# Optimization experiments

Measured on AMD Instinct MI355X. Metric: run time of the kernel, lower is better.

Reference implementation:

```python
import jax, jax.numpy as jnp
import numpy as np

HEAD_SIZE = 64

def setup_inputs() -> dict:
    key = jax.random.key(0)
    k1, k2, k3, k4 = jax.random.split(key, 4)
    B, T, D = 4, 4096, 768
    x = jax.random.normal(k1, (B, T, D), dtype=jnp.float32)
    Wq = jax.random.normal(k2, (D, HEAD_SIZE), dtype=jnp.float32) * (1.0 / np.sqrt(D))
    Wk = jax.random.normal(k3, (D, HEAD_SIZE), dtype=jnp.float32) * (1.0 / np.sqrt(D))
    Wv = jax.random.normal(k4, (D, HEAD_SIZE), dtype=jnp.float32) * (1.0 / np.sqrt(D))
    return {"x": x, "Wq": Wq, "Wk": Wk, "Wv": Wv}

def reference(x, Wq, Wk, Wv):
    # q,k,v: [B, T, H]
    q = jnp.einsum('btd,dh->bth', x, Wq)
    k = jnp.einsum('btd,dh->bth', x, Wk)
    v = jnp.einsum('btd,dh->bth', x, Wv)
    # scores: [B, T, T]; causal mask via lower-triangular band, -inf elsewhere
    scores = jnp.einsum('bqh,bkh->bqk', q, k)
    T = x.shape[1]
    causal = jnp.tril(jnp.ones((T, T), dtype=bool))  # band_part(ones, -1, 0)
    scores = jnp.where(causal[None, :, :], scores, -jnp.inf)
    attn = jax.nn.softmax(scores / np.sqrt(HEAD_SIZE), axis=-1)
    # dropout is identity in eval mode
    return jnp.einsum('bqk,bkh->bqh', attn, v)
```

## Files before the change

kernel.cpp:

```cpp
#include <hip/hip_runtime.h>
#include <math.h>

typedef __attribute__((ext_vector_type(8))) short short8;
typedef __attribute__((ext_vector_type(4))) float f32x4;
typedef unsigned short ushort_t;

#define TSEQ   4096
#define NBATCH 4
#define DMODEL 768
#define HS     64
#define KSPLIT 8

static __device__ __forceinline__ ushort_t f2bf(float f) {
  union { float f; unsigned u; } v; v.f = f;
  unsigned r = v.u + 0x7fffu + ((v.u >> 16) & 1u);
  return (ushort_t)(r >> 16);
}
static __device__ __forceinline__ float bf2f(ushort_t u) {
  union { unsigned u; float f; } v; v.u = ((unsigned)u) << 16; return v.f;
}

#define MFMA16(a,b,c) __builtin_amdgcn_mfma_f32_16x16x32_bf16((a),(b),(c),0,0,0)

__global__ __launch_bounds__(256) void wprep(
    const float* __restrict__ Wq, const float* __restrict__ Wk,
    const float* __restrict__ Wv, ushort_t* __restrict__ Wt)
{
  __shared__ float lds[64 * 65];
  const int m = blockIdx.x / 12, kc = blockIdx.x % 12, k0 = kc * 64;
  const float* W = (m == 0) ? Wq : (m == 1) ? Wk : Wv;
  const int tid = threadIdx.x;
#pragma unroll
  for (int i = 0; i < 16; i++) {
    const int row = i * 4 + (tid >> 6), col = tid & 63;
    lds[row * 65 + col] = W[(size_t)(k0 + row) * HS + col];
  }
  __syncthreads();
#pragma unroll
  for (int i = 0; i < 16; i++) {
    const int n = i * 4 + (tid >> 6), kk = tid & 63;
    Wt[(size_t)(m * 64 + n) * DMODEL + k0 + kk] = f2bf(lds[kk * 65 + n]);
  }
}

__global__ __launch_bounds__(512, 1) void qkv_mfma(
    const float* __restrict__ x, const ushort_t* __restrict__ Wt,
    ushort_t* __restrict__ q, ushort_t* __restrict__ kO, ushort_t* __restrict__ vT)
{
  __shared__ __align__(16) ushort_t sA[2][64 * 72];
  __shared__ __align__(16) ushort_t sB[2][192 * 64];

  const int tid  = threadIdx.x;
  const int w    = tid >> 6;
  const int wm   = w >> 2, wn = w & 3;
  const int lane = tid & 63;
  const int l16  = lane & 15, quad = lane >> 4;
  const int M0   = blockIdx.x * 64;

  const int arow = tid >> 3, acol = (tid & 7) * 8;
  const float* ax = x + (size_t)(M0 + arow) * DMODEL + acol;

  const int bcol_l = lane >> 3;
  const int bkoff  = (((lane & 7) ^ (bcol_l & 7)) << 3);

  f32x4 acc[2][3];
#pragma unroll
  for (int mt = 0; mt < 2; mt++)
#pragma unroll
    for (int nt = 0; nt < 3; nt++) acc[mt][nt] = (f32x4){0.f, 0.f, 0.f, 0.f};

  {
#pragma unroll
    for (int j = 0; j < 3; j++) {
      const int colb = w * 24 + j * 8;
      __builtin_amdgcn_global_load_lds(
          (const __attribute__((address_space(1))) ushort_t*)
              (Wt + (size_t)(colb + bcol_l) * DMODEL + bkoff),
          (__attribute__((address_space(3))) ushort_t*)(&sB[0][colb * 64]),
          16, 0, 0);
    }
    const float4 f0 = *(const float4*)(ax);
    const float4 f1 = *(const float4*)(ax + 4);
    short8 p;
    p[0]=f2bf(f0.x); p[1]=f2bf(f0.y); p[2]=f2bf(f0.z); p[3]=f2bf(f0.w);
    p[4]=f2bf(f1.x); p[5]=f2bf(f1.y); p[6]=f2bf(f1.z); p[7]=f2bf(f1.w);
    *(short8*)(&sA[0][arow * 72 + acol]) = p;
  }

  for (int ks = 0; ks < DMODEL / 64; ks++) {
    const int cur = ks & 1, nxt = cur ^ 1;
    __syncthreads();

    float4 f0n, f1n;
    if (ks < DMODEL / 64 - 1) {
#pragma unroll
      for (int j = 0; j < 3; j++) {
        const int colb = w * 24 + j * 8;
        __builtin_amdgcn_global_load_lds(
            (const __attribute__((address_space(1))) ushort_t*)
                (Wt + (size_t)(colb + bcol_l) * DMODEL + (ks + 1) * 64 + bkoff),
            (__attribute__((address_space(3))) ushort_t*)(&sB[nxt][colb * 64]),
            16, 0, 0);
      }
      f0n = *(const float4*)(ax + (ks + 1) * 64);
      f1n = *(const float4*)(ax + (ks + 1) * 64 + 4);
    }

    const ushort_t* sAc = &sA[cur][0];
    const ushort_t* sBc = &sB[cur][0];
#pragma unroll
    for (int kc = 0; kc < 2; kc++) {
      const short8 a0 = *(const short8*)(sAc + (wm * 32 + l16)      * 72 + kc * 32 + quad * 8);
      const short8 a1 = *(const short8*)(sAc + (wm * 32 + 16 + l16) * 72 + kc * 32 + quad * 8);
      const int kswz = (kc * 32 + quad * 8) ^ ((l16 & 7) << 3);
#pragma unroll
      for (int nt = 0; nt < 3; nt++) {
        const short8 bf =
            *(const short8*)(sBc + (wn * 48 + nt * 16 + l16) * 64 + kswz);
        acc[0][nt] = MFMA16(a0, bf, acc[0][nt]);
        acc[1][nt] = MFMA16(a1, bf, acc[1][nt]);
      }
    }

    if (ks < DMODEL / 64 - 1) {
      short8 p;
      p[0]=f2bf(f0n.x); p[1]=f2bf(f0n.y); p[2]=f2bf(f0n.z); p[3]=f2bf(f0n.w);
      p[4]=f2bf(f1n.x); p[5]=f2bf(f1n.y); p[6]=f2bf(f1n.z); p[7]=f2bf(f1n.w);
      *(short8*)(&sA[nxt][arow * 72 + acol]) = p;
    }
  }

#pragma unroll
  for (int mt = 0; mt < 2; mt++)
#pragma unroll
    for (int nt = 0; nt < 3; nt++) {
      const int gnt = wn * 3 + nt;
      const int mat = gnt >> 2;
      if (mat == 0) {
        const int col = (gnt & 3) * 16 + l16;
#pragma unroll
        for (int r = 0; r < 4; r++)
          q[(size_t)(M0 + wm * 32 + mt * 16 + quad * 4 + r) * HS + col] =
              f2bf(acc[mt][nt][r] * 0.125f);
      } else if (mat == 1) {
        const int cb2 = (gnt & 3) * 2 + (l16 >> 3);
#pragma unroll
        for (int r = 0; r < 4; r++) {
          const int trow  = M0 + wm * 32 + mt * 16 + quad * 4 + r;
          const int cphys = ((cb2 ^ (trow & 7)) << 3) | (l16 & 7);
          kO[(size_t)trow * HS + cphys] = f2bf(acc[mt][nt][r]);
        }
      }
    }
  __syncthreads();
  float* vls = (float*)&sA[0][0];
#pragma unroll
  for (int mt = 0; mt < 2; mt++)
#pragma unroll
    for (int nt = 0; nt < 3; nt++) {
      const int gnt = wn * 3 + nt;
      if ((gnt >> 2) == 2) {
        const int vcol = (gnt & 3) * 16 + l16;
#pragma unroll
        for (int r = 0; r < 4; r++)
          vls[(wm * 32 + mt * 16 + quad * 4 + r) * 65 + vcol] = acc[mt][nt][r];
      }
    }
  __syncthreads();
  const int d = tid >> 3, seg = tid & 7;
  short8 pk;
#pragma unroll
  for (int i = 0; i < 8; i++) pk[i] = (short)f2bf(vls[(seg * 8 + i) * 65 + d]);
  {
    const int tb  = M0 & (TSEQ - 1);
    const int kbp = seg ^ (d & 7);
    *(short8*)(vT + ((size_t)(M0 >> 12) * HS + d) * TSEQ + tb + kbp * 8) = pk;
  }
}

__global__ __launch_bounds__(256, 4) void attn_part(
    const ushort_t* __restrict__ q, const ushort_t* __restrict__ k,
    const ushort_t* __restrict__ vT, float* __restrict__ ML, ushort_t* __restrict__ OP)
{
  __shared__ __align__(16) ushort_t sK[2][64 * 64];
  __shared__ __align__(16) ushort_t sV[2][64 * 64];
  __shared__ __align__(16) ushort_t sP[4][16 * 64];

  const int idx  = blockIdx.x;
  const int s    = idx & 7;
  const int b    = (idx >> 3) & 3;
  const int jp   = idx >> 5;
  const int tid  = threadIdx.x;
  const int w    = tid >> 6;
  const int lane = tid & 63;
  const int l16  = lane & 15, quad = lane >> 4;

  const ushort_t* qg = q  + (size_t)b * TSEQ * HS;
  const ushort_t* kg = k  + (size_t)b * TSEQ * HS;
  const ushort_t* vg = vT + (size_t)b * HS * TSEQ;

  const int srow = lane >> 3;
  const int scol = (lane & 7) * 8;

#pragma unroll
  for (int h = 0; h < 2; h++) {
    const int j  = h ? jp : (63 - jp);
    const int R0 = j * 64 + w * 16;

    const short8 qf0 = *(const short8*)(qg + (size_t)(R0 + l16) * HS +      quad * 8);
    const short8 qf1 = *(const short8*)(qg + (size_t)(R0 + l16) * HS + 32 + quad * 8);

    f32x4 o[4];
#pragma unroll
    for (int dt = 0; dt < 4; dt++) o[dt] = (f32x4){0.f, 0.f, 0.f, 0.f};
    float mrow = -INFINITY, lrow = 0.f;

    const int nkt = j + 1;
    int kt = s, cur = 0;
    if (h) __syncthreads();
    if (kt < nkt) {
      const int k0 = kt * 64;
#pragma unroll
      for (int jj = 0; jj < 2; jj++) {
        const int r0 = w * 16 + jj * 8;
        __builtin_amdgcn_global_load_lds(
            (const __attribute__((address_space(1))) ushort_t*)
                (kg + (size_t)(k0 + r0 + srow) * HS + scol),
            (__attribute__((address_space(3))) ushort_t*)(&sK[0][r0 * 64]),
            16, 0, 0);
        __builtin_amdgcn_global_load_lds(
            (const __attribute__((address_space(1))) ushort_t*)
                (vg + (size_t)(r0 + srow) * TSEQ + k0 + scol),
            (__attribute__((address_space(3))) ushort_t*)(&sV[0][r0 * 64]),
            16, 0, 0);
      }
    }
    for (; kt < nkt; kt += KSPLIT) {
      const int k0 = kt * 64;
      __syncthreads();
      if (kt + KSPLIT < nkt) {
        const int kn = (kt + KSPLIT) * 64;
#pragma unroll
        for (int jj = 0; jj < 2; jj++) {
          const int r0 = w * 16 + jj * 8;
          __builtin_amdgcn_global_load_lds(
              (const __attribute__((address_space(1))) ushort_t*)
                  (kg + (size_t)(kn + r0 + srow) * HS + scol),
              (__attribute__((address_space(3))) ushort_t*)(&sK[cur ^ 1][r0 * 64]),
              16, 0, 0);
          __builtin_amdgcn_global_load_lds(
              (const __attribute__((address_space(1))) ushort_t*)
                  (vg + (size_t)(r0 + srow) * TSEQ + kn + scol),
              (__attribute__((address_space(3))) ushort_t*)(&sV[cur ^ 1][r0 * 64]),
              16, 0, 0);
        }
      }
      const ushort_t* sKc = &sK[cur][0];
      const ushort_t* sVc = &sV[cur][0];
      const int sw = (l16 & 7) << 3;

      f32x4 sT[4];
      __builtin_amdgcn_s_setprio(1);
#pragma unroll
      for (int ct = 0; ct < 4; ct++) {
        sT[ct] = (f32x4){0.f, 0.f, 0.f, 0.f};
        const short8 kfa = *(const short8*)(sKc + (ct * 16 + l16) * 64 + ((quad * 8)      ^ sw));
        const short8 kfb = *(const short8*)(sKc + (ct * 16 + l16) * 64 + ((32 + quad * 8) ^ sw));
        sT[ct] = MFMA16(kfa, qf0, sT[ct]);
        sT[ct] = MFMA16(kfb, qf1, sT[ct]);
      }
      __builtin_amdgcn_s_setprio(0);
      if (k0 + 63 > R0) {
        const int qrow = R0 + l16;
#pragma unroll
        for (int ct = 0; ct < 4; ct++)
#pragma unroll
          for (int r = 0; r < 4; r++)
            sT[ct][r] = (k0 + ct * 16 + quad * 4 + r <= qrow) ? sT[ct][r] : -INFINITY;
      }
      float tm = -INFINITY;
#pragma unroll
      for (int ct = 0; ct < 4; ct++)
#pragma unroll
        for (int r = 0; r < 4; r++) tm = fmaxf(tm, sT[ct][r]);
      tm = fmaxf(tm, __shfl_xor(tm, 16));
      tm = fmaxf(tm, __shfl_xor(tm, 32));
      const float mn = fmaxf(mrow, tm);
      const float al = __expf(mrow - mn);
      mrow = mn;
      float ps = 0.f;
#pragma unroll
      for (int ct = 0; ct < 4; ct++)
#pragma unroll
        for (int r = 0; r < 4; r++) { sT[ct][r] = __expf(sT[ct][r] - mn); ps += sT[ct][r]; }
      ps += __shfl_xor(ps, 16);
      ps += __shfl_xor(ps, 32);
      lrow = lrow * al + ps;
      ushort_t* Pw = &sP[w][0];
#pragma unroll
      for (int ct = 0; ct < 4; ct++) {
        ushort4 pk;
        pk.x = f2bf(sT[ct][0]); pk.y = f2bf(sT[ct][1]);
        pk.z = f2bf(sT[ct][2]); pk.w = f2bf(sT[ct][3]);
        const int pb = (ct * 2 + (quad >> 1)) ^ (l16 & 7);
        *(ushort4*)(Pw + l16 * 64 + pb * 8 + (quad & 1) * 4) = pk;
      }
      float alo[4];
#pragma unroll
      for (int r = 0; r < 4; r++) alo[r] = __shfl(al, quad * 4 + r);
#pragma unroll
      for (int dt = 0; dt < 4; dt++)
#pragma unroll
        for (int r = 0; r < 4; r++) o[dt][r] *= alo[r];
      const short8 pf0 = *(const short8*)(Pw + l16 * 64 + (((quad)     ^ (l16 & 7)) << 3));
      const short8 pf1 = *(const short8*)(Pw + l16 * 64 + (((4 + quad) ^ (l16 & 7)) << 3));
      __builtin_amdgcn_s_setprio(1);
#pragma unroll
      for (int dt = 0; dt < 4; dt++) {
        const short8 vfa = *(const short8*)(sVc + (dt * 16 + l16) * 64 + ((quad * 8)      ^ sw));
        const short8 vfb = *(const short8*)(sVc + (dt * 16 + l16) * 64 + ((32 + quad * 8) ^ sw));
        o[dt] = MFMA16(pf0, vfa, o[dt]);
        o[dt] = MFMA16(pf1, vfb, o[dt]);
      }
      __builtin_amdgcn_s_setprio(0);
      cur ^= 1;
    }

    const size_t base = ((size_t)(b * KSPLIT + s) * TSEQ);
    if (quad == 0) {
      ML[(base + R0 + l16) * 2 + 0] = mrow;
      ML[(base + R0 + l16) * 2 + 1] = lrow;
    }
#pragma unroll
    for (int dt = 0; dt < 4; dt++)
#pragma unroll
      for (int r = 0; r < 4; r++)
        OP[(base + R0 + quad * 4 + r) * HS + dt * 16 + l16] = f2bf(o[dt][r]);
  }
}

__global__ __launch_bounds__(256) void attn_merge(
    const float* __restrict__ ML, const ushort_t* __restrict__ OP,
    float* __restrict__ out)
{
  const int row = blockIdx.x * 32 + (threadIdx.x >> 3);
  const int b   = row >> 12, t = row & (TSEQ - 1);
  const int d0  = (threadIdx.x & 7) * 8;
  float m[KSPLIT], l[KSPLIT];
  float M = -INFINITY;
#pragma unroll
  for (int ss = 0; ss < KSPLIT; ss++) {
    const size_t i = ((size_t)(b * KSPLIT + ss) * TSEQ + t);
    m[ss] = ML[i * 2]; l[ss] = ML[i * 2 + 1];
    M = fmaxf(M, m[ss]);
  }
  float den = 0.f;
  float n0=0.f,n1=0.f,n2=0.f,n3=0.f,n4=0.f,n5=0.f,n6=0.f,n7=0.f;
#pragma unroll
  for (int ss = 0; ss < KSPLIT; ss++) {
    const float a = __expf(m[ss] - M);
    den += l[ss] * a;
    const size_t i = ((size_t)(b * KSPLIT + ss) * TSEQ + t);
    const short8 u = *(const short8*)(OP + i * HS + d0);
    n0 += a * bf2f((ushort_t)u[0]); n1 += a * bf2f((ushort_t)u[1]);
    n2 += a * bf2f((ushort_t)u[2]); n3 += a * bf2f((ushort_t)u[3]);
    n4 += a * bf2f((ushort_t)u[4]); n5 += a * bf2f((ushort_t)u[5]);
    n6 += a * bf2f((ushort_t)u[6]); n7 += a * bf2f((ushort_t)u[7]);
  }
  const float inv = 1.f / den;
  float* op = out + (size_t)row * HS + d0;
  *(float4*)(op)     = make_float4(n0 * inv, n1 * inv, n2 * inv, n3 * inv);
  *(float4*)(op + 4) = make_float4(n4 * inv, n5 * inv, n6 * inv, n7 * inv);
}

extern "C" void kernel_launch(void* const* d_in, const int* in_sizes, int n_in,
                              void* d_out, int out_size, void* d_ws, size_t ws_size,
                              hipStream_t stream) {
  const float* x  = (const float*)d_in[0];
  const float* Wq = (const float*)d_in[1];
  const float* Wk = (const float*)d_in[2];
  const float* Wv = (const float*)d_in[3];
  float* out = (float*)d_out;

  char* ws = (char*)d_ws;
  ushort_t* Wt = (ushort_t*)ws;
  ushort_t* qb = (ushort_t*)(ws + 294912);
  ushort_t* kb = (ushort_t*)(ws + 294912 + 2097152);
  ushort_t* vb = (ushort_t*)(ws + 294912 + 2 * 2097152);
  float*    ml = (float*)   (ws + 294912 + 3 * 2097152);
  ushort_t* op = (ushort_t*)(ws + 294912 + 3 * 2097152 + 1048576);

  wprep<<<36, 256, 0, stream>>>(Wq, Wk, Wv, Wt);
  qkv_mfma<<<(NBATCH * TSEQ) / 64, 512, 0, stream>>>(x, Wt, qb, kb, vb);
  attn_part<<<32 * NBATCH * KSPLIT, 256, 0, stream>>>(qb, kb, vb, ml, op);
  attn_merge<<<512, 256, 0, stream>>>(ml, op, out);
}
```

Measured before the change: 128.5 us.

## Process two 64-row query groups per block to reuse each K/V tile

Each attention block now handles a 128-row query tile, split into two 64-row groups, and applies every staged K/V tile in LDS to both groups. Global K/V traffic and tile staging per query row roughly halve, and the grid shrinks to half as many blocks. In exchange the kernel holds twice the accumulator and Q registers and twice the P scratch, and occupancy is lowered to 3 waves per SIMD. Fewer blocks may also leave CUs idle or load-imbalanced.

New measurement: 132.2 us. +2.9%, slower.

```diff
diff --git a/kernel.cpp b/kernel.cpp
--- a/kernel.cpp
+++ b/kernel.cpp
@@ -178,13 +178,13 @@
   }
 }
 
-__global__ __launch_bounds__(256, 4) void attn_part(
+__global__ __launch_bounds__(256, 3) void attn_part(
     const ushort_t* __restrict__ q, const ushort_t* __restrict__ k,
     const ushort_t* __restrict__ vT, float* __restrict__ ML, ushort_t* __restrict__ OP)
 {
   __shared__ __align__(16) ushort_t sK[2][64 * 64];
   __shared__ __align__(16) ushort_t sV[2][64 * 64];
-  __shared__ __align__(16) ushort_t sP[4][16 * 64];
+  __shared__ __align__(16) ushort_t sP[4][2][16 * 64];
 
   const int idx  = blockIdx.x;
   const int s    = idx & 7;
@@ -204,18 +204,26 @@
 
 #pragma unroll
   for (int h = 0; h < 2; h++) {
-    const int j  = h ? jp : (63 - jp);
-    const int R0 = j * 64 + w * 16;
-
-    const short8 qf0 = *(const short8*)(qg + (size_t)(R0 + l16) * HS +      quad * 8);
-    const short8 qf1 = *(const short8*)(qg + (size_t)(R0 + l16) * HS + 32 + quad * 8);
-
-    f32x4 o[4];
-#pragma unroll
-    for (int dt = 0; dt < 4; dt++) o[dt] = (f32x4){0.f, 0.f, 0.f, 0.f};
-    float mrow = -INFINITY, lrow = 0.f;
-
-    const int nkt = j + 1;
+    const int j  = h ? jp : (31 - jp);
+    const int TB = j * 128;
+
+    short8 qf[2][2];
+#pragma unroll
+    for (int g = 0; g < 2; g++) {
+      const int R0g = TB + g * 64 + w * 16;
+      qf[g][0] = *(const short8*)(qg + (size_t)(R0g + l16) * HS +      quad * 8);
+      qf[g][1] = *(const short8*)(qg + (size_t)(R0g + l16) * HS + 32 + quad * 8);
+    }
+
+    f32x4 o[2][4];
+#pragma unroll
+    for (int g = 0; g < 2; g++)
+#pragma unroll
+      for (int dt = 0; dt < 4; dt++) o[g][dt] = (f32x4){0.f, 0.f, 0.f, 0.f};
+    float mrow[2] = {-INFINITY, -INFINITY};
+    float lrow[2] = {0.f, 0.f};
+
+    const int nkt = 2 * j + 2;
     int kt = s, cur = 0;
     if (h) __syncthreads();
     if (kt < nkt) {
@@ -259,83 +267,93 @@
       const ushort_t* sVc = &sV[cur][0];
       const int sw = (l16 & 7) << 3;
 
-      f32x4 sT[4];
-      __builtin_amdgcn_s_setprio(1);
-#pragma unroll
-      for (int ct = 0; ct < 4; ct++) {
-        sT[ct] = (f32x4){0.f, 0.f, 0.f, 0.f};
-        const short8 kfa = *(const short8*)(sKc + (ct * 16 + l16) * 64 + ((quad * 8)      ^ sw));
-        const short8 kfb = *(const short8*)(sKc + (ct * 16 + l16) * 64 + ((32 + quad * 8) ^ sw));
-        sT[ct] = MFMA16(kfa, qf0, sT[ct]);
-        sT[ct] = MFMA16(kfb, qf1, sT[ct]);
-      }
-      __builtin_amdgcn_s_setprio(0);
-      if (k0 + 63 > R0) {
-        const int qrow = R0 + l16;
+#pragma unroll
+      for (int g = 0; g < 2; g++) {
+        if (k0 > TB + g * 64 + 63) continue;
+        const int R0g = TB + g * 64 + w * 16;
+
+        f32x4 sT[4];
+        __builtin_amdgcn_s_setprio(1);
+#pragma unroll
+        for (int ct = 0; ct < 4; ct++) {
+          sT[ct] = (f32x4){0.f, 0.f, 0.f, 0.f};
+          const short8 kfa = *(const short8*)(sKc + (ct * 16 + l16) * 64 + ((quad * 8)      ^ sw));
+          const short8 kfb = *(const short8*)(sKc + (ct * 16 + l16) * 64 + ((32 + quad * 8) ^ sw));
+          sT[ct] = MFMA16(kfa, qf[g][0], sT[ct]);
+          sT[ct] = MFMA16(kfb, qf[g][1], sT[ct]);
+        }
+        __builtin_amdgcn_s_setprio(0);
+        if (k0 + 63 > R0g) {
+          const int qrow = R0g + l16;
+#pragma unroll
+          for (int ct = 0; ct < 4; ct++)
+#pragma unroll
+            for (int r = 0; r < 4; r++)
+              sT[ct][r] = (k0 + ct * 16 + quad * 4 + r <= qrow) ? sT[ct][r] : -INFINITY;
+        }
+        float tm = -INFINITY;
 #pragma unroll
         for (int ct = 0; ct < 4; ct++)
 #pragma unroll
-          for (int r = 0; r < 4; r++)
-            sT[ct][r] = (k0 + ct * 16 + quad * 4 + r <= qrow) ? sT[ct][r] : -INFINITY;
-      }
-      float tm = -INFINITY;
-#pragma unroll
-      for (int ct = 0; ct < 4; ct++)
-#pragma unroll
-        for (int r = 0; r < 4; r++) tm = fmaxf(tm, sT[ct][r]);
-      tm = fmaxf(tm, __shfl_xor(tm, 16));
-      tm = fmaxf(tm, __shfl_xor(tm, 32));
-      const float mn = fmaxf(mrow, tm);
-      const float al = __expf(mrow - mn);
-      mrow = mn;
-      float ps = 0.f;
-#pragma unroll
-      for (int ct = 0; ct < 4; ct++)
-#pragma unroll
-        for (int r = 0; r < 4; r++) { sT[ct][r] = __expf(sT[ct][r] - mn); ps += sT[ct][r]; }
-      ps += __shfl_xor(ps, 16);
-      ps += __shfl_xor(ps, 32);
-      lrow = lrow * al + ps;
-      ushort_t* Pw = &sP[w][0];
-#pragma unroll
-      for (int ct = 0; ct < 4; ct++) {
-        ushort4 pk;
-        pk.x = f2bf(sT[ct][0]); pk.y = f2bf(sT[ct][1]);
-        pk.z = f2bf(sT[ct][2]); pk.w = f2bf(sT[ct][3]);
-        const int pb = (ct * 2 + (quad >> 1)) ^ (l16 & 7);
-        *(ushort4*)(Pw + l16 * 64 + pb * 8 + (quad & 1) * 4) = pk;
-      }
-      float alo[4];
-#pragma unroll
-      for (int r = 0; r < 4; r++) alo[r] = __shfl(al, quad * 4 + r);
+          for (int r = 0; r < 4; r++) tm = fmaxf(tm, sT[ct][r]);
+        tm = fmaxf(tm, __shfl_xor(tm, 16));
+        tm = fmaxf(tm, __shfl_xor(tm, 32));
+        const float mn = fmaxf(mrow[g], tm);
+        const float al = __expf(mrow[g] - mn);
+        mrow[g] = mn;
+        float ps = 0.f;
+#pragma unroll
+        for (int ct = 0; ct < 4; ct++)
+#pragma unroll
+          for (int r = 0; r < 4; r++) { sT[ct][r] = __expf(sT[ct][r] - mn); ps += sT[ct][r]; }
+        ps += __shfl_xor(ps, 16);
+        ps += __shfl_xor(ps, 32);
+        lrow[g] = lrow[g] * al + ps;
+        ushort_t* Pw = &sP[w][g][0];
+#pragma unroll
+        for (int ct = 0; ct < 4; ct++) {
+          ushort4 pk;
+          pk.x = f2bf(sT[ct][0]); pk.y = f2bf(sT[ct][1]);
+          pk.z = f2bf(sT[ct][2]); pk.w = f2bf(sT[ct][3]);
+          const int pb = (ct * 2 + (quad >> 1)) ^ (l16 & 7);
+          *(ushort4*)(Pw + l16 * 64 + pb * 8 + (quad & 1) * 4) = pk;
+        }
+        float alo[4];
+#pragma unroll
+        for (int r = 0; r < 4; r++) alo[r] = __shfl(al, quad * 4 + r);
+#pragma unroll
+        for (int dt = 0; dt < 4; dt++)
+#pragma unroll
+          for (int r = 0; r < 4; r++) o[g][dt][r] *= alo[r];
+        const short8 pf0 = *(const short8*)(Pw + l16 * 64 + (((quad)     ^ (l16 & 7)) << 3));
+        const short8 pf1 = *(const short8*)(Pw + l16 * 64 + (((4 + quad) ^ (l16 & 7)) << 3));
+        __builtin_amdgcn_s_setprio(1);
+#pragma unroll
+        for (int dt = 0; dt < 4; dt++) {
+          const short8 vfa = *(const short8*)(sVc + (dt * 16 + l16) * 64 + ((quad * 8)      ^ sw));
+          const short8 vfb = *(const short8*)(sVc + (dt * 16 + l16) * 64 + ((32 + quad * 8) ^ sw));
+          o[g][dt] = MFMA16(pf0, vfa, o[g][dt]);
+          o[g][dt] = MFMA16(pf1, vfb, o[g][dt]);
+        }
+        __builtin_amdgcn_s_setprio(0);
+      }
+      cur ^= 1;
+    }
+
+    const size_t base = ((size_t)(b * KSPLIT + s) * TSEQ);
+#pragma unroll
+    for (int g = 0; g < 2; g++) {
+      const int R0g = TB + g * 64 + w * 16;
+      if (quad == 0) {
+        ML[(base + R0g + l16) * 2 + 0] = mrow[g];
+        ML[(base + R0g + l16) * 2 + 1] = lrow[g];
+      }
 #pragma unroll
       for (int dt = 0; dt < 4; dt++)
 #pragma unroll
-        for (int r = 0; r < 4; r++) o[dt][r] *= alo[r];
-      const short8 pf0 = *(const short8*)(Pw + l16 * 64 + (((quad)     ^ (l16 & 7)) << 3));
-      const short8 pf1 = *(const short8*)(Pw + l16 * 64 + (((4 + quad) ^ (l16 & 7)) << 3));
-      __builtin_amdgcn_s_setprio(1);
-#pragma unroll
-      for (int dt = 0; dt < 4; dt++) {
-        const short8 vfa = *(const short8*)(sVc + (dt * 16 + l16) * 64 + ((quad * 8)      ^ sw));
-        const short8 vfb = *(const short8*)(sVc + (dt * 16 + l16) * 64 + ((32 + quad * 8) ^ sw));
-        o[dt] = MFMA16(pf0, vfa, o[dt]);
-        o[dt] = MFMA16(pf1, vfb, o[dt]);
-      }
-      __builtin_amdgcn_s_setprio(0);
-      cur ^= 1;
-    }
-
-    const size_t base = ((size_t)(b * KSPLIT + s) * TSEQ);
-    if (quad == 0) {
-      ML[(base + R0 + l16) * 2 + 0] = mrow;
-      ML[(base + R0 + l16) * 2 + 1] = lrow;
-    }
-#pragma unroll
-    for (int dt = 0; dt < 4; dt++)
-#pragma unroll
-      for (int r = 0; r < 4; r++)
-        OP[(base + R0 + quad * 4 + r) * HS + dt * 16 + l16] = f2bf(o[dt][r]);
+        for (int r = 0; r < 4; r++)
+          OP[(base + R0g + quad * 4 + r) * HS + dt * 16 + l16] = f2bf(o[g][dt][r]);
+    }
   }
 }
 
@@ -392,6 +410,6 @@
 
   wprep<<<36, 256, 0, stream>>>(Wq, Wk, Wv, Wt);
   qkv_mfma<<<(NBATCH * TSEQ) / 64, 512, 0, stream>>>(x, Wt, qb, kb, vb);
-  attn_part<<<32 * NBATCH * KSPLIT, 256, 0, stream>>>(qb, kb, vb, ml, op);
+  attn_part<<<16 * NBATCH * KSPLIT, 256, 0, stream>>>(qb, kb, vb, ml, op);
   attn_merge<<<512, 256, 0, stream>>>(ml, op, out);
 }
```
